# Kernel tuning notes

Measured on AMD Instinct MI355X. Metric: run time of the kernel, lower is better.

## Reference

```python
import jax, jax.numpy as jnp
import numpy as np

N_TAU = 100  # number of steps per delay interval: dt = tau / N_TAU = 0.01 * tau


def _F(x, y, t, params):
    # Delay-logistic vector field: x'(t) = theta0 * x(t) * (1 - theta1 * x(t - tau))
    return params[0] * x * (1.0 - params[1] * y)


def setup_inputs() -> dict:
    key = jax.random.key(0)
    k1, = jax.random.split(key, 1)
    d = 32768
    x_0 = jax.random.uniform(k1, (d,), dtype=jnp.float32)  # positive ICs, stable dynamics
    tau = jnp.ones((1,), dtype=jnp.float32)
    params = jnp.ones((2,), dtype=jnp.float32)  # theta0, theta1
    N = 1000  # T = N * dt = 10 * tau
    return {"x_0": x_0, "tau": tau, "params": params, "N": N}


def reference(x_0, tau, params, N):
    # Forward-Euler DDE solve with constant history x(t) = x_0 for t in [-tau, 0].
    d = x_0.shape[0]
    dt = 0.01 * tau[0]
    dtype = x_0.dtype
    traj0 = jnp.zeros((N + 1, d), dtype=dtype).at[0].set(x_0)  # rows are time steps

    def step(traj, i):
        x_i = traj[i]                                            # current state [d]
        # delayed state x(t_i - tau): history (= x_0) for the first N_TAU steps
        y_i = jnp.where(i >= N_TAU, traj[jnp.maximum(i - N_TAU, 0)], x_0)
        t_i = i.astype(dtype) * dt
        x_next = x_i + dt * _F(x_i, y_i, t_i, params)
        return traj.at[i + 1].set(x_next), None

    traj, _ = jax.lax.scan(step, traj0, jnp.arange(N))
    # match torch convention: kth COLUMN is the state at the kth time step -> [d, N+1]
    return traj.T
```

## Files before the change

### kernel.cpp

```cpp
#include <hip/hip_runtime.h>


constexpr int NT   = 1000;
constexpr int NTAU = 100;
constexpr int NGRP = NT / NTAU;
constexpr int NP1  = NT + 1;
constexpr int CPB  = 64;
constexpr int HW   = 50;
constexpr int LSTR = HW + 1;

#define R5(F,B)   F(B) F((B)+1) F((B)+2) F((B)+3) F((B)+4)
#define R25(F,B)  R5(F,B) R5(F,(B)+5) R5(F,(B)+10) R5(F,(B)+15) R5(F,(B)+20)
#define R50(F,B)  R25(F,B) R25(F,(B)+25)
#define R100(F)   R50(F,0) R50(F,50)

#define LDS_ORDER() do {                                    \
    __builtin_amdgcn_sched_barrier(0);                      \
    asm volatile("s_waitcnt lgkmcnt(0)" ::: "memory");      \
    __builtin_amdgcn_sched_barrier(0);                      \
} while (0)

__global__ __launch_bounds__(CPB, 1)
void ndde_kernel(const float* __restrict__ x0,
                 const float* __restrict__ tau,
                 const float* __restrict__ params,
                 float* __restrict__ out)
{
    __shared__ float lds[CPB][LSTR];
    const int tid = threadIdx.x;
    const int g = (NGRP - 1) - (int)blockIdx.y;
    const long long jbase = (long long)blockIdx.x * CPB;

    const float dt = 0.01f * tau[0];
    const float a  = dt * params[0];
    const float q  = -(a * params[1]);
    const float p  = 1.0f + a;

    float x = x0[jbase + tid];
    float h[NTAU];
#define INIT_H(K) h[(K)] = x;
    R100(INIT_H)

#define STEP(K) { const float y_ = h[(K)]; h[(K)] = x; x *= fmaf(q, y_, p); }
#pragma clang loop unroll(disable)
    for (int gg = 0; gg <= g; ++gg) {
        R100(STEP)
    }

    const long long t0 = (long long)g * NTAU;
    float* gp0 = out + jbase * NP1 + t0 + tid;

#define STG_A(K) lds[tid][(K)] = h[(K)];
    R50(STG_A, 0)
    LDS_ORDER();
    if (tid < HW) {
#pragma unroll 8
        for (int r = 0; r < CPB; ++r)
            gp0[(long long)r * NP1] = lds[r][tid];
    }
    LDS_ORDER();

#define STG_B(K) lds[tid][(K)] = h[50+(K)];
    R50(STG_B, 0)
    LDS_ORDER();
    if (tid < HW) {
        float* gpB = gp0 + HW;
#pragma unroll 8
        for (int r = 0; r < CPB; ++r)
            gpB[(long long)r * NP1] = lds[r][tid];
    }

    if (g == NGRP - 1)
        out[(jbase + tid) * NP1 + NT] = x;
}

extern "C" void kernel_launch(void* const* d_in, const int* in_sizes, int n_in,
                              void* d_out, int out_size, void* d_ws, size_t ws_size,
                              hipStream_t stream) {
    const float* x0     = (const float*)d_in[0];
    const float* tau    = (const float*)d_in[1];
    const float* params = (const float*)d_in[2];
    float* out = (float*)d_out;
    const int d = in_sizes[0];
    const int chunks = d / CPB;
    dim3 grid(chunks, NGRP);
    ndde_kernel<<<grid, CPB, 0, stream>>>(x0, tau, params, out);
}
```

Measured before the change: 38.38 us.

## Stream all time groups from one block instead of recomputing per group

Each block previously covered one 100-step output group and recomputed the recurrence from t=0 up to that group, which is redundant work across 10 blocks per column chunk. Now a single block per chunk walks all groups in order, writing each group through LDS right after computing it. This removes the recomputation but cuts the grid to 512 single-wave blocks, so parallelism drops and each block runs a longer serial chain of compute and stores.

```diff
diff --git a/kernel.cpp b/kernel.cpp
--- a/kernel.cpp
+++ b/kernel.cpp
@@ -6,8 +6,7 @@
 constexpr int NGRP = NT / NTAU;
 constexpr int NP1  = NT + 1;
 constexpr int CPB  = 64;
-constexpr int HW   = 50;
-constexpr int LSTR = HW + 1;
+constexpr int LSTR = NTAU + 1;
 
 #define R5(F,B)   F(B) F((B)+1) F((B)+2) F((B)+3) F((B)+4)
 #define R25(F,B)  R5(F,B) R5(F,(B)+5) R5(F,(B)+10) R5(F,(B)+15) R5(F,(B)+20)
@@ -28,7 +27,6 @@
 {
     __shared__ float lds[CPB][LSTR];
     const int tid = threadIdx.x;
-    const int g = (NGRP - 1) - (int)blockIdx.y;
     const long long jbase = (long long)blockIdx.x * CPB;
 
     const float dt = 0.01f * tau[0];
@@ -41,37 +39,28 @@
 #define INIT_H(K) h[(K)] = x;
     R100(INIT_H)
 
+    float* rowbase = out + jbase * NP1;
+
 #define STEP(K) { const float y_ = h[(K)]; h[(K)] = x; x *= fmaf(q, y_, p); }
+#define STG(K)  lds[tid][(K)] = h[(K)];
+
 #pragma clang loop unroll(disable)
-    for (int gg = 0; gg <= g; ++gg) {
+    for (int g = 0; g < NGRP; ++g) {
         R100(STEP)
+        R100(STG)
+        LDS_ORDER();
+
+        float* gp = rowbase + g * NTAU + tid;
+#pragma unroll 4
+        for (int r = 0; r < CPB; ++r) {
+            gp[(long long)r * NP1] = lds[r][tid];
+            if (tid < NTAU - 64)
+                gp[(long long)r * NP1 + 64] = lds[r][64 + tid];
+        }
+        LDS_ORDER();
     }
 
-    const long long t0 = (long long)g * NTAU;
-    float* gp0 = out + jbase * NP1 + t0 + tid;
-
-#define STG_A(K) lds[tid][(K)] = h[(K)];
-    R50(STG_A, 0)
-    LDS_ORDER();
-    if (tid < HW) {
-#pragma unroll 8
-        for (int r = 0; r < CPB; ++r)
-            gp0[(long long)r * NP1] = lds[r][tid];
-    }
-    LDS_ORDER();
-
-#define STG_B(K) lds[tid][(K)] = h[50+(K)];
-    R50(STG_B, 0)
-    LDS_ORDER();
-    if (tid < HW) {
-        float* gpB = gp0 + HW;
-#pragma unroll 8
-        for (int r = 0; r < CPB; ++r)
-            gpB[(long long)r * NP1] = lds[r][tid];
-    }
-
-    if (g == NGRP - 1)
-        out[(jbase + tid) * NP1 + NT] = x;
+    out[(jbase + tid) * NP1 + NT] = x;
 }
 
 extern "C" void kernel_launch(void* const* d_in, const int* in_sizes, int n_in,
@@ -82,7 +71,6 @@
     const float* params = (const float*)d_in[2];
     float* out = (float*)d_out;
     const int d = in_sizes[0];
-    const int chunks = d / CPB;
-    dim3 grid(chunks, NGRP);
-    ndde_kernel<<<grid, CPB, 0, stream>>>(x0, tau, params, out);
+    const int nblocks = d / CPB;
+    ndde_kernel<<<nblocks, CPB, 0, stream>>>(x0, tau, params, out);
 }
```

After: 53.74 us. +40.0%, slower.

## Split delay history between registers and an LDS ring to cut VGPR use

Applied to the files above, without the earlier changes.

The 100-entry delay buffer is split so that 72 entries stay in registers and 28 live in an LDS ring. The LDS part is written out directly as the final tail segment, and the register part is staged in three chunks of 24. Index math also moves from 64-bit to 32-bit. The aim is to lower register pressure and reuse LDS for the history. In exchange, LDS loads and stores now sit on the serial recurrence chain, which adds latency to each step.

```diff
diff --git a/kernel.cpp b/kernel.cpp
--- a/kernel.cpp
+++ b/kernel.cpp
@@ -6,13 +6,20 @@
 constexpr int NGRP = NT / NTAU;
 constexpr int NP1  = NT + 1;
 constexpr int CPB  = 64;
-constexpr int HW   = 50;
-constexpr int LSTR = HW + 1;
+constexpr int RREG = 72;
+constexpr int RLDS = 28;
+constexpr int LSTR = RLDS + 1;
+constexpr int PH   = 24;
 
+#define R2(F,B)   F(B) F((B)+1)
+#define R4(F,B)   R2(F,B) R2(F,(B)+2)
 #define R5(F,B)   F(B) F((B)+1) F((B)+2) F((B)+3) F((B)+4)
-#define R25(F,B)  R5(F,B) R5(F,(B)+5) R5(F,(B)+10) R5(F,(B)+15) R5(F,(B)+20)
+#define R20(F,B)  R5(F,B) R5(F,(B)+5) R5(F,(B)+10) R5(F,(B)+15)
+#define R24(F,B)  R20(F,B) R4(F,(B)+20)
+#define R25(F,B)  R20(F,B) R5(F,(B)+20)
+#define R28(F,B)  R25(F,B) F((B)+25) F((B)+26) F((B)+27)
 #define R50(F,B)  R25(F,B) R25(F,(B)+25)
-#define R100(F)   R50(F,0) R50(F,50)
+#define R72(F)    R50(F,0) R20(F,50) R2(F,70)
 
 #define LDS_ORDER() do {                                    \
     __builtin_amdgcn_sched_barrier(0);                      \
@@ -26,10 +33,10 @@
                  const float* __restrict__ params,
                  float* __restrict__ out)
 {
-    __shared__ float lds[CPB][LSTR];
+    __shared__ float ring[CPB][LSTR];
     const int tid = threadIdx.x;
     const int g = (NGRP - 1) - (int)blockIdx.y;
-    const long long jbase = (long long)blockIdx.x * CPB;
+    const int jbase = (int)blockIdx.x * CPB;
 
     const float dt = 0.01f * tau[0];
     const float a  = dt * params[0];
@@ -37,37 +44,63 @@
     const float p  = 1.0f + a;
 
     float x = x0[jbase + tid];
-    float h[NTAU];
+    float h[RREG];
 #define INIT_H(K) h[(K)] = x;
-    R100(INIT_H)
+    R72(INIT_H)
+#define INIT_L(K) ring[tid][(K)] = x;
+    R28(INIT_L, 0)
 
-#define STEP(K) { const float y_ = h[(K)]; h[(K)] = x; x *= fmaf(q, y_, p); }
+#define STEP_R(K) { const float y_ = h[(K)];         h[(K)] = x;         x *= fmaf(q, y_, p); }
+#define STEP_L(K) { const float y_ = ring[tid][(K)]; ring[tid][(K)] = x; x *= fmaf(q, y_, p); }
+
 #pragma clang loop unroll(disable)
     for (int gg = 0; gg <= g; ++gg) {
-        R100(STEP)
+        R72(STEP_R)
+        R28(STEP_L, 0)
     }
 
-    const long long t0 = (long long)g * NTAU;
-    float* gp0 = out + jbase * NP1 + t0 + tid;
+    const int obase = jbase * NP1 + g * NTAU;
 
-#define STG_A(K) lds[tid][(K)] = h[(K)];
-    R50(STG_A, 0)
     LDS_ORDER();
-    if (tid < HW) {
+    if (tid < RLDS) {
+        float* gp = out + obase + RREG + tid;
 #pragma unroll 8
         for (int r = 0; r < CPB; ++r)
-            gp0[(long long)r * NP1] = lds[r][tid];
+            gp[r * NP1] = ring[r][tid];
     }
     LDS_ORDER();
 
-#define STG_B(K) lds[tid][(K)] = h[50+(K)];
-    R50(STG_B, 0)
+#define STG0(K) ring[tid][(K)] = h[(K)];
+#define STG1(K) ring[tid][(K)] = h[24+(K)];
+#define STG2(K) ring[tid][(K)] = h[48+(K)];
+
+    R24(STG0, 0)
     LDS_ORDER();
-    if (tid < HW) {
-        float* gpB = gp0 + HW;
+    if (tid < PH) {
+        float* gp = out + obase + 0 * PH + tid;
 #pragma unroll 8
         for (int r = 0; r < CPB; ++r)
-            gpB[(long long)r * NP1] = lds[r][tid];
+            gp[r * NP1] = ring[r][tid];
+    }
+    LDS_ORDER();
+
+    R24(STG1, 0)
+    LDS_ORDER();
+    if (tid < PH) {
+        float* gp = out + obase + 1 * PH + tid;
+#pragma unroll 8
+        for (int r = 0; r < CPB; ++r)
+            gp[r * NP1] = ring[r][tid];
+    }
+    LDS_ORDER();
+
+    R24(STG2, 0)
+    LDS_ORDER();
+    if (tid < PH) {
+        float* gp = out + obase + 2 * PH + tid;
+#pragma unroll 8
+        for (int r = 0; r < CPB; ++r)
+            gp[r * NP1] = ring[r][tid];
     }
 
     if (g == NGRP - 1)
```

Result: slower. 45.61 us (+18.8%).
